# Performance work log

Measured on AMD Instinct MI355X. Metric: run time of the kernel, lower is better.

The kernel has to match this reference:

```python
import jax, jax.numpy as jnp
import numpy as np

B, NF, S, L, H, MID, KS, NC, DENSE = 16, 8, 16, 256, 128, 32, 8, 10, 512
COEFF = 0.1
BN_EPS = 1e-5


def _normalize(x):
    return x / jnp.maximum(jnp.linalg.norm(x, axis=-1, keepdims=True), 1e-12)


def _sparsemax(z):
    # sparsemax over last axis (Martins & Astudillo 2016)
    zs = jnp.flip(jnp.sort(z, axis=-1), axis=-1)
    k = jnp.arange(1, z.shape[-1] + 1, dtype=z.dtype)
    cum = jnp.cumsum(zs, axis=-1)
    support = (1.0 + k * zs) > cum
    ksup = jnp.sum(support, axis=-1, keepdims=True)
    tau = (jnp.take_along_axis(cum, ksup - 1, axis=-1) - 1.0) / ksup.astype(z.dtype)
    return jnp.maximum(z - tau, 0.0)


def _bn_ncl(x, g, b, m, v):  # eval-mode BatchNorm1d on [N, C, L]
    return g[None, :, None] * (x - m[None, :, None]) * jax.lax.rsqrt(v[None, :, None] + BN_EPS) + b[None, :, None]


def _bn_nc(x, g, b, m, v):  # eval-mode BatchNorm1d on [N, C]
    return g * (x - m) * jax.lax.rsqrt(v + BN_EPS) + b


def _conv(x, w, pad):
    return jax.lax.conv_general_dilated(x, w, (1,), [(pad, pad)], dimension_numbers=('NCH', 'OIH', 'NCH'))


def _maxpool2(x):  # MaxPool1d(kernel=2, stride=2, padding=1): -inf padded
    return jax.lax.reduce_window(x, -jnp.inf, jax.lax.max, (1, 1, 2), (1, 1, 2), ((0, 0), (0, 0), (1, 1)))


def _cnn(x, cw1, bn1, cw2, bn2, cw3, bn3):
    x = _maxpool2(jax.nn.relu(_bn_ncl(_conv(x, cw1, KS // 2), *bn1)))
    x = _maxpool2(jax.nn.relu(_bn_ncl(_conv(x, cw2, 4), *bn2)))
    x = _maxpool2(jax.nn.relu(_bn_ncl(_conv(x, cw3, 4), *bn3)))
    return jnp.mean(x, axis=-1)  # AdaptiveAvgPool1d(1) -> [N, H]


def _alpha_beta(x, cw1, bn1, cw2, bn2, cw3, bn3, Wq, bq, Wk, bk, Wv, bv):
    b = x.shape[0]
    xf = jnp.transpose(x, (1, 0, 2, 3)).reshape(NF, b * S, 1, L)
    rep = jax.vmap(_cnn)(xf, cw1, bn1, cw2, bn2, cw3, bn3)  # [F, B*S, H]
    rep = rep.reshape(NF, b, S, H)
    Q = jax.nn.elu(rep @ Wq + bq)
    K = jax.nn.leaky_relu(rep @ Wk + bk)
    V = jax.nn.leaky_relu(rep @ Wv + bv)
    # mean_t(Q @ K^T) == Q @ mean_t(K); then scale by sqrt(d_k)
    scores = jnp.einsum('fbsh,fbh->fbs', Q, jnp.mean(K, axis=2)) / jnp.sqrt(jnp.float32(H))
    intra_aw = _sparsemax(scores)                             # [F, B, S]
    Z = _normalize(jnp.einsum('fbs,fbsh->fbh', intra_aw, V))  # [F, B, H]
    Kn = _normalize(rep)
    inter_scores = jnp.einsum('ibh,fbsh->ifbs', Z, Kn)        # cosine scores (Z already unit-norm)
    inter_aw = _sparsemax(inter_scores)                       # [I, F, B, S]
    U = jnp.einsum('ifbs,fbsh->ibh', inter_aw, rep) / NF      # mean over feature axis f
    Hc = _normalize(jnp.concatenate([Z, U], axis=-1))         # [F, B, 2H]
    feat = jnp.transpose(Hc, (1, 0, 2)).reshape(b, NF * 2 * H)
    return feat, intra_aw, inter_aw


def _forward(src_x, src_y, tgt_x, cw1, bn1_g, bn1_b, bn1_m, bn1_v, cw2, bn2_g, bn2_b, bn2_m, bn2_v, cw3, bn3_g, bn3_b, bn3_m, bn3_v, Wq, bq, Wk, bk, Wv, bv, bnc1_g, bnc1_b, bnc1_m, bnc1_v, W1, b1, bnc2_g, bnc2_b, bnc2_m, bnc2_v, W2, b2):
    bn1 = (bn1_g, bn1_b, bn1_m, bn1_v)
    bn2 = (bn2_g, bn2_b, bn2_m, bn2_v)
    bn3 = (bn3_g, bn3_b, bn3_m, bn3_v)
    sf, sa, sb = _alpha_beta(src_x, cw1, bn1, cw2, bn2, cw3, bn3, Wq, bq, Wk, bk, Wv, bv)
    _, ta, tb = _alpha_beta(tgt_x, cw1, bn1, cw2, bn2, cw3, bn3, Wq, bq, Wk, bk, Wv, bv)
    h = _bn_nc(sf, bnc1_g, bnc1_b, bnc1_m, bnc1_v) @ W1 + b1
    h = jax.nn.leaky_relu(_bn_nc(h, bnc2_g, bnc2_b, bnc2_m, bnc2_v))
    y_pred = jax.nn.softmax(h @ W2 + b2, axis=-1)
    # MMD domain losses (detached in original via torch.tensor(list))
    da = jnp.mean(sa - ta, axis=-2)                           # [F, S]
    loss_a = COEFF * jnp.mean(jnp.linalg.norm(da, axis=-1))
    db = jnp.mean(sb - tb, axis=-2)                           # [I, F, S]
    loss_b = COEFF * jnp.mean(jnp.sqrt(jnp.sum(db * db, axis=(1, 2))))
    dom = jax.lax.stop_gradient(loss_a + loss_b)
    # CrossEntropyLoss applied to already-softmaxed preds, as in source
    logp = jax.nn.log_softmax(y_pred, axis=-1)
    ce = -jnp.mean(logp[jnp.arange(y_pred.shape[0]), src_y])
    return y_pred, ce + dom


def setup_inputs() -> dict:
    ks = jax.random.split(jax.random.key(0), 40)
    rn = lambda i, sh, s=1.0: s * jax.random.normal(ks[i], sh, dtype=jnp.float32)
    ru = lambda i, sh, lo, hi: jax.random.uniform(ks[i], sh, jnp.float32, lo, hi)
    return {
        'src_x': rn(0, (B, NF, S, L)),
        'src_y': jax.random.randint(ks[1], (B,), 0, NC),
        'tgt_x': rn(2, (B, NF, S, L)),
        'cw1': rn(3, (NF, MID, 1, KS), 0.1),
        'bn1_g': ru(4, (NF, MID), 0.75, 1.25), 'bn1_b': rn(5, (NF, MID), 0.1),
        'bn1_m': rn(6, (NF, MID), 0.1), 'bn1_v': ru(7, (NF, MID), 0.5, 1.5),
        'cw2': rn(8, (NF, 2 * MID, MID, 8), 0.05),
        'bn2_g': ru(9, (NF, 2 * MID), 0.75, 1.25), 'bn2_b': rn(10, (NF, 2 * MID), 0.1),
        'bn2_m': rn(11, (NF, 2 * MID), 0.1), 'bn2_v': ru(12, (NF, 2 * MID), 0.5, 1.5),
        'cw3': rn(13, (NF, H, 2 * MID, 8), 0.05),
        'bn3_g': ru(14, (NF, H), 0.75, 1.25), 'bn3_b': rn(15, (NF, H), 0.1),
        'bn3_m': rn(16, (NF, H), 0.1), 'bn3_v': ru(17, (NF, H), 0.5, 1.5),
        'Wq': rn(18, (H, H), 0.05), 'bq': rn(19, (H,), 0.02),
        'Wk': rn(20, (H, H), 0.05), 'bk': rn(21, (H,), 0.02),
        'Wv': rn(22, (H, H), 0.05), 'bv': rn(23, (H,), 0.02),
        'bnc1_g': ru(24, (NF * 2 * H,), 0.75, 1.25), 'bnc1_b': rn(25, (NF * 2 * H,), 0.1),
        'bnc1_m': rn(26, (NF * 2 * H,), 0.1), 'bnc1_v': ru(27, (NF * 2 * H,), 0.5, 1.5),
        'W1': rn(28, (NF * 2 * H, DENSE), 0.03), 'b1': rn(29, (DENSE,), 0.02),
        'bnc2_g': ru(30, (DENSE,), 0.75, 1.25), 'bnc2_b': rn(31, (DENSE,), 0.1),
        'bnc2_m': rn(32, (DENSE,), 0.1), 'bnc2_v': ru(33, (DENSE,), 0.5, 1.5),
        'W2': rn(34, (DENSE, NC), 0.05), 'b2': rn(35, (NC,), 0.02),
    }


def reference(src_x, src_y, tgt_x, cw1, bn1_g, bn1_b, bn1_m, bn1_v, cw2, bn2_g, bn2_b, bn2_m, bn2_v, cw3, bn3_g, bn3_b, bn3_m, bn3_v, Wq, bq, Wk, bk, Wv, bv, bnc1_g, bnc1_b, bnc1_m, bnc1_v, W1, b1, bnc2_g, bnc2_b, bnc2_m, bnc2_v, W2, b2):
    return _forward(src_x, src_y, tgt_x, cw1, bn1_g, bn1_b, bn1_m, bn1_v, cw2, bn2_g, bn2_b, bn2_m, bn2_v, cw3, bn3_g, bn3_b, bn3_m, bn3_v, Wq, bq, Wk, bk, Wv, bv, bnc1_g, bnc1_b, bnc1_m, bnc1_v, W1, b1, bnc2_g, bnc2_b, bnc2_m, bnc2_v, W2, b2)
```

## Files before the change

### kernel.cpp

```cpp
#include <hip/hip_runtime.h>

typedef unsigned short u16;
typedef unsigned int u32;
typedef __attribute__((ext_vector_type(8))) short bfrag;
typedef __attribute__((ext_vector_type(4))) float ffrag;

__device__ __forceinline__ float lrelu(float x) { return x >= 0.f ? x : 0.01f * x; }
__device__ __forceinline__ float eluf(float x)  { return x > 0.f ? x : expm1f(x); }
__device__ __forceinline__ u16 f2bf(float f) {
    u32 x = __float_as_uint(f);
    return (u16)((x + 0x7fffu + ((x >> 16) & 1u)) >> 16);
}
__device__ __forceinline__ u16 f2bt(float f) {
    return (u16)(__float_as_uint(f) >> 16);
}
__device__ __forceinline__ float bf2f(u16 u) {
    return __uint_as_float(((u32)u) << 16);
}

__device__ void sparsemax16(const float* z, float* out) {
    float zs[16];
    for (int i = 0; i < 16; ++i) zs[i] = z[i];
    for (int i = 1; i < 16; ++i) {
        float key = zs[i]; int j = i - 1;
        while (j >= 0 && zs[j] < key) { zs[j + 1] = zs[j]; --j; }
        zs[j + 1] = key;
    }
    float cum[16];
    cum[0] = zs[0];
    for (int i = 1; i < 16; ++i) cum[i] = cum[i - 1] + zs[i];
    int ksup = 0;
    for (int k = 1; k <= 16; ++k)
        if (1.0f + (float)k * zs[k - 1] > cum[k - 1]) ksup++;
    if (ksup < 1) ksup = 1;
    float tau = (cum[ksup - 1] - 1.0f) / (float)ksup;
    for (int i = 0; i < 16; ++i) out[i] = fmaxf(z[i] - tau, 0.0f);
}

__global__ __launch_bounds__(256) void k_wprep(
    const float* __restrict__ w2, const float* __restrict__ w3,
    const float* __restrict__ Wq, const float* __restrict__ Wk,
    const float* __restrict__ Wv,
    u16* __restrict__ wpk2, u16* __restrict__ wpk3, u16* __restrict__ wqkv)
{
    int i = blockIdx.x * 256 + threadIdx.x;
    if (i < 131072) {
        int j = i & 7, L = (i >> 3) & 63, kc = (i >> 9) & 7, nt = (i >> 12) & 3, f = i >> 14;
        int co = nt * 16 + (L & 15);
        int ci = ((L >> 4) << 3) + j;
        wpk2[i] = f2bf(w2[(((size_t)f * 64 + co) * 32 + ci) * 8 + kc]);
    } else if (i < 131072 + 524288) {
        int i2 = i - 131072;
        int j = i2 & 7, L = (i2 >> 3) & 63, kc = (i2 >> 9) & 15, nt = (i2 >> 13) & 7, f = i2 >> 16;
        int co = nt * 16 + (L & 15);
        int ci = ((kc & 1) << 5) + ((L >> 4) << 3) + j;
        wpk3[i2] = f2bf(w3[(((size_t)f * 128 + co) * 64 + ci) * 8 + (kc >> 1)]);
    } else if (i < 131072 + 524288 + 49152) {
        int j2 = i - 655360;
        int proj = j2 >> 14, idx = j2 & 16383;
        int jj = idx & 7, L = (idx >> 3) & 63, kc = (idx >> 9) & 3, nt = idx >> 11;
        int n = nt * 16 + (L & 15);
        int k = kc * 32 + ((L >> 4) << 3) + jj;
        const float* W = proj == 0 ? Wq : (proj == 1 ? Wk : Wv);
        wqkv[j2] = f2bf(W[k * 128 + n]);
    }
}

#define S1T_STRIDE 40
#define S2T_STRIDE 72
#define RB2_STRIDE 68
#define RB3_STRIDE 140
#define RB_OFF 6336
#define SMEM_U16 (RB_OFF + 67 * RB3_STRIDE)

__global__ __launch_bounds__(256) void k_cnn(
    const float* __restrict__ xs, const float* __restrict__ xt,
    const float* __restrict__ w1, const float* __restrict__ g1, const float* __restrict__ b1,
    const float* __restrict__ m1, const float* __restrict__ v1,
    const float* __restrict__ g2, const float* __restrict__ b2,
    const float* __restrict__ m2, const float* __restrict__ v2,
    const float* __restrict__ g3, const float* __restrict__ b3,
    const float* __restrict__ m3, const float* __restrict__ v3,
    const u16* __restrict__ wpk2, const u16* __restrict__ wpk3,
    float* __restrict__ rep)
{
    __shared__ __align__(16) u16 smem[SMEM_U16];
    float* xin = (float*)(smem + RB_OFF);

    int tid = threadIdx.x, blk = blockIdx.x;
    int pass = blk >> 11, f = (blk >> 8) & 7, n = blk & 255;
    int bb = n >> 4, ss = n & 15;
    int lane = tid & 63, w = tid >> 6;
    const float* x = pass ? xt : xs;
    float* rep_p = rep + (size_t)pass * 262144;

    {
        u32* z = (u32*)smem;
        for (int i = tid; i < 80; i += 256) z[i] = 0;
        for (int i = tid; i < 360; i += 256) z[2660 + i] = 0;
        if (tid < 4) { xin[tid] = 0.f; xin[260 + tid] = 0.f; }
        const float* xr = x + (((size_t)bb * 8 + f) * 16 + ss) * 256;
        for (int i = tid; i < 256; i += 256) xin[i + 4] = xr[i];
    }
    __syncthreads();

    if (tid < 208) {
        int cc = tid & 7, jc = tid >> 3;
        int co0 = cc * 4, j0 = jc * 5;
        float wr[4][8];
        for (int c = 0; c < 4; ++c) {
            const float4* q = reinterpret_cast<const float4*>(w1 + ((size_t)f * 32 + co0 + c) * 8);
            float4 a = q[0], bq = q[1];
            wr[c][0] = a.x; wr[c][1] = a.y; wr[c][2] = a.z; wr[c][3] = a.w;
            wr[c][4] = bq.x; wr[c][5] = bq.y; wr[c][6] = bq.z; wr[c][7] = bq.w;
        }
        int px[10];
        for (int i = 0; i < 10; ++i) {
            int p = 2 * j0 - 1 + i;
            px[i] = p < 0 ? 0 : (p > 256 ? 256 : p);
        }
        float acc[4][10];
        for (int c = 0; c < 4; ++c) for (int i = 0; i < 10; ++i) acc[c][i] = 0.f;
        for (int k = 0; k < 8; ++k) {
            float xv[10];
            for (int i = 0; i < 10; ++i) xv[i] = xin[px[i] + k];
            for (int c = 0; c < 4; ++c)
                for (int i = 0; i < 10; ++i) acc[c][i] += wr[c][k] * xv[i];
        }
        for (int c = 0; c < 4; ++c) {
            int co = co0 + c;
            float sc = g1[f * 32 + co] * rsqrtf(v1[f * 32 + co] + 1e-5f);
            float sh = b1[f * 32 + co] - m1[f * 32 + co] * sc;
            for (int jj = 0; jj < 5; ++jj) {
                int j = j0 + jj;
                if (j < 129) {
                    float a0 = fmaxf(acc[c][2 * jj] * sc + sh, 0.f);
                    float a1 = fmaxf(acc[c][2 * jj + 1] * sc + sh, 0.f);
                    smem[(j + 4) * S1T_STRIDE + co] = f2bt(fmaxf(a0, a1));
                }
            }
        }
    }
    __syncthreads();

    {
        int nt = w;
        bfrag B2[8];
        const bfrag* gB = reinterpret_cast<const bfrag*>(wpk2);
        for (int kc = 0; kc < 8; ++kc)
            B2[kc] = gB[(((size_t)f * 4 + nt) * 8 + kc) * 64 + lane];
        int co = nt * 16 + (lane & 15);
        float sc = g2[f * 64 + co] * rsqrtf(v2[f * 64 + co] + 1e-5f);
        float sh = b2[f * 64 + co] - m2[f * 64 + co] * sc;
        int arow = lane & 15, ci0 = (lane >> 4) << 3;
        for (int mt = 0; mt < 9; ++mt) {
            ffrag C = {0.f, 0.f, 0.f, 0.f};
            int rb = mt * 16 + arow;
            for (int kc = 0; kc < 8; ++kc) {
                bfrag A = *reinterpret_cast<const bfrag*>(&smem[(rb + kc) * S1T_STRIDE + ci0]);
                C = __builtin_amdgcn_mfma_f32_16x16x32_bf16(A, B2[kc], C, 0, 0, 0);
            }
            int p0 = mt * 16 + ((lane >> 4) << 2);
            for (int r = 0; r < 4; ++r) {
                int p = p0 + r;
                if (p < 130)
                    smem[RB_OFF + p * RB2_STRIDE + co] = f2bt(fmaxf(C[r] * sc + sh, 0.f));
            }
        }
    }
    __syncthreads();

    {
        u32* z = (u32*)smem;
        for (int i = tid; i < 144; i += 256) z[i] = 0;
        for (int i = tid; i < 612; i += 256) z[2520 + i] = 0;
    }
    for (int e = tid; e < 66 * 64; e += 256) {
        int j = e >> 6, ci = e & 63;
        float vmax;
        if (j == 0) {
            vmax = bf2f(smem[RB_OFF + 0 * RB2_STRIDE + ci]);
        } else if (j == 65) {
            vmax = bf2f(smem[RB_OFF + 129 * RB2_STRIDE + ci]);
        } else {
            float a0 = bf2f(smem[RB_OFF + (2 * j - 1) * RB2_STRIDE + ci]);
            float a1 = bf2f(smem[RB_OFF + (2 * j) * RB2_STRIDE + ci]);
            vmax = fmaxf(a0, a1);
        }
        smem[(j + 4) * S2T_STRIDE + ci] = f2bt(vmax);
    }
    __syncthreads();

    for (int t = 0; t < 2; ++t) {
        int nt = w * 2 + t;
        bfrag B3[16];
        const bfrag* gB = reinterpret_cast<const bfrag*>(wpk3);
        for (int kc = 0; kc < 16; ++kc)
            B3[kc] = gB[(((size_t)f * 8 + nt) * 16 + kc) * 64 + lane];
        int co = nt * 16 + (lane & 15);
        float sc = g3[f * 128 + co] * rsqrtf(v3[f * 128 + co] + 1e-5f);
        float sh = b3[f * 128 + co] - m3[f * 128 + co] * sc;
        int arow = lane & 15, q8 = (lane >> 4) << 3;
        for (int mt = 0; mt < 5; ++mt) {
            ffrag C = {0.f, 0.f, 0.f, 0.f};
            int rb = mt * 16 + arow;
            for (int kc = 0; kc < 16; ++kc) {
                int row = rb + (kc >> 1);
                int ci0 = ((kc & 1) << 5) + q8;
                bfrag A = *reinterpret_cast<const bfrag*>(&smem[row * S2T_STRIDE + ci0]);
                C = __builtin_amdgcn_mfma_f32_16x16x32_bf16(A, B3[kc], C, 0, 0, 0);
            }
            int p0 = mt * 16 + ((lane >> 4) << 2);
            for (int r = 0; r < 4; ++r) {
                int p = p0 + r;
                if (p < 67)
                    smem[RB_OFF + p * RB3_STRIDE + co] = f2bt(fmaxf(C[r] * sc + sh, 0.f));
            }
        }
    }
    __syncthreads();

    if (tid < 128) {
        int co = tid;
        float sum = bf2f(smem[RB_OFF + 0 * RB3_STRIDE + co]);
        for (int j = 1; j < 34; ++j) {
            float a0 = bf2f(smem[RB_OFF + (2 * j - 1) * RB3_STRIDE + co]);
            float a1 = bf2f(smem[RB_OFF + (2 * j) * RB3_STRIDE + co]);
            sum += fmaxf(a0, a1);
        }
        rep_p[(((size_t)f * 256) + n) * 128 + co] = sum * (1.0f / 34.0f);
    }
}

__global__ __launch_bounds__(256) void k_attn1(
    const float* __restrict__ rep, const u16* __restrict__ wqkv,
    const float* __restrict__ bq, const float* __restrict__ bk,
    const float* __restrict__ bv,
    float* __restrict__ Zn, float* __restrict__ rninv, float* __restrict__ iaw)
{
    __shared__ __align__(16) u16 repbf[16 * 136];
    __shared__ float KmL[128], ZL[128], awL[16], scoresL[16], r2L[16];
    __shared__ float spart[4][4][4];
    __shared__ float redL[4];
    int tid = threadIdx.x;
    int pass = blockIdx.x >> 7, f = (blockIdx.x >> 4) & 7, b = blockIdx.x & 15;
    const float* rp = rep + (size_t)pass * 262144 + ((size_t)f * 256 + b * 16) * 128;
    float* Zn_p = Zn + (size_t)pass * 16384;
    float* rninv_p = rninv + (size_t)pass * 2048;
    float* iaw_p = iaw + (size_t)pass * 2048;

    {
        int s = tid >> 4, i = tid & 15, h0 = i * 8;
        const float4* q4 = reinterpret_cast<const float4*>(rp + s * 128 + h0);
        float4 a = q4[0], c = q4[1];
        float p2 = a.x*a.x + a.y*a.y + a.z*a.z + a.w*a.w
                 + c.x*c.x + c.y*c.y + c.z*c.z + c.w*c.w;
        bfrag pk;
        pk[0] = (short)f2bt(a.x); pk[1] = (short)f2bt(a.y);
        pk[2] = (short)f2bt(a.z); pk[3] = (short)f2bt(a.w);
        pk[4] = (short)f2bt(c.x); pk[5] = (short)f2bt(c.y);
        pk[6] = (short)f2bt(c.z); pk[7] = (short)f2bt(c.w);
        *reinterpret_cast<bfrag*>(&repbf[s * 136 + h0]) = pk;
        p2 += __shfl_xor(p2, 1); p2 += __shfl_xor(p2, 2);
        p2 += __shfl_xor(p2, 4); p2 += __shfl_xor(p2, 8);
        if (i == 0) r2L[s] = p2;
    }
    __syncthreads();

    int lane = tid & 63, w = tid >> 6, arow = lane & 15, q = lane >> 4;
    bfrag A[4];
    for (int kc = 0; kc < 4; ++kc)
        A[kc] = *reinterpret_cast<const bfrag*>(&repbf[arow * 136 + kc * 32 + q * 8]);

    float qv[2][4], vvv[2][4];
    int colv[2];
    const bfrag* BB = reinterpret_cast<const bfrag*>(wqkv);
    for (int t = 0; t < 2; ++t) {
        int nt = w * 2 + t;
        ffrag cq = {0.f,0.f,0.f,0.f}, ck = {0.f,0.f,0.f,0.f}, cv = {0.f,0.f,0.f,0.f};
        for (int kc = 0; kc < 4; ++kc) {
            int fi = (nt * 4 + kc) * 64 + lane;
            bfrag Bq = BB[fi];
            bfrag Bk = BB[2048 + fi];
            bfrag Bv = BB[4096 + fi];
            cq = __builtin_amdgcn_mfma_f32_16x16x32_bf16(A[kc], Bq, cq, 0, 0, 0);
            ck = __builtin_amdgcn_mfma_f32_16x16x32_bf16(A[kc], Bk, ck, 0, 0, 0);
            cv = __builtin_amdgcn_mfma_f32_16x16x32_bf16(A[kc], Bv, cv, 0, 0, 0);
        }
        int col = nt * 16 + arow;
        colv[t] = col;
        float bqc = bq[col], bkc = bk[col], bvc = bv[col];
        float kpt = 0.f;
        for (int r = 0; r < 4; ++r) {
            qv[t][r] = eluf(cq[r] + bqc);
            vvv[t][r] = lrelu(cv[r] + bvc);
            kpt += lrelu(ck[r] + bkc);
        }
        kpt += __shfl_xor(kpt, 16);
        kpt += __shfl_xor(kpt, 32);
        if (q == 0) KmL[col] = kpt * (1.f / 16.f);
    }
    __syncthreads();

    {
        float km0 = KmL[colv[0]], km1 = KmL[colv[1]];
        float ps[4];
        for (int r = 0; r < 4; ++r) {
            float v = qv[0][r] * km0 + qv[1][r] * km1;
            v += __shfl_xor(v, 1); v += __shfl_xor(v, 2);
            v += __shfl_xor(v, 4); v += __shfl_xor(v, 8);
            ps[r] = v;
        }
        if (arow == 0)
            for (int r = 0; r < 4; ++r) spart[w][q][r] = ps[r];
    }
    __syncthreads();
    if (tid < 16) {
        int qq = tid >> 2, rr = tid & 3;
        float sc = spart[0][qq][rr] + spart[1][qq][rr] + spart[2][qq][rr] + spart[3][qq][rr];
        scoresL[tid] = sc * 0.08838834764831845f;
        rninv_p[f * 256 + b * 16 + tid] = 1.f / fmaxf(sqrtf(r2L[tid]), 1e-12f);
    }
    __syncthreads();
    if (tid == 0) sparsemax16(scoresL, awL);
    __syncthreads();
    if (tid < 16) iaw_p[f * 256 + b * 16 + tid] = awL[tid];

    for (int t = 0; t < 2; ++t) {
        float zp = 0.f;
        for (int r = 0; r < 4; ++r) zp += awL[q * 4 + r] * vvv[t][r];
        zp += __shfl_xor(zp, 16);
        zp += __shfl_xor(zp, 32);
        if (q == 0) ZL[colv[t]] = zp;
    }
    __syncthreads();
    if (tid < 128) {
        float z = ZL[tid];
        float v = z * z;
        v += __shfl_xor(v, 1); v += __shfl_xor(v, 2); v += __shfl_xor(v, 4);
        v += __shfl_xor(v, 8); v += __shfl_xor(v, 16); v += __shfl_xor(v, 32);
        if (lane == 0) redL[w] = v;
    }
    __syncthreads();
    if (tid == 0) redL[2] = 1.f / fmaxf(sqrtf(redL[0] + redL[1]), 1e-12f);
    __syncthreads();
    if (tid < 128)
        Zn_p[((size_t)f * 16 + b) * 128 + tid] = ZL[tid] * redL[2];
}

__global__ __launch_bounds__(256) void k_attn2(
    const float* __restrict__ rep, const float* __restrict__ Zn,
    const float* __restrict__ rninv, float* __restrict__ ibw,
    const float* __restrict__ g, const float* __restrict__ bb,
    const float* __restrict__ mm, const float* __restrict__ vv,
    float* __restrict__ featbn)
{
    __shared__ float repL[16384];
    __shared__ float ZiL[128], scores[128], UL[128];
    __shared__ float awLf[8][16];
    __shared__ float redL[2];
    int tid = threadIdx.x, blk = blockIdx.x;
    int pass = blk >> 7, b = (blk >> 3) & 15, i = blk & 7;
    const float* rep_p = rep + (size_t)pass * 262144;

    for (int f = 0; f < 8; ++f) {
        const float4* src = reinterpret_cast<const float4*>(
            rep_p + ((size_t)f * 256 + b * 16) * 128);
        float4* dst = reinterpret_cast<float4*>(repL + f * 2048);
        for (int t = tid; t < 512; t += 256) dst[t] = src[t];
    }
    if (tid < 128) ZiL[tid] = Zn[(size_t)pass * 16384 + ((size_t)i * 16 + b) * 128 + tid];
    __syncthreads();

    if (tid < 128) {
        int f = tid >> 4, s = tid & 15;
        const float* rr = repL + tid * 128;
        float a = 0.f;
        for (int h = 0; h < 128; ++h) a += ZiL[h] * rr[h];
        scores[tid] = a * rninv[(size_t)pass * 2048 + f * 256 + b * 16 + s];
    }
    __syncthreads();
    if (tid < 8) {
        float aw[16];
        sparsemax16(&scores[tid * 16], aw);
        for (int s = 0; s < 16; ++s) awLf[tid][s] = aw[s];
    }
    __syncthreads();
    if (tid < 128) {
        int f = tid >> 4, s = tid & 15;
        ibw[(size_t)pass * 16384 + (((size_t)i * 8 + f) * 16 + b) * 16 + s] = awLf[f][s];
    }
    if (pass == 0) {
        if (tid < 128) {
            int h = tid;
            float u = 0.f;
            for (int f = 0; f < 8; ++f) {
                const float* rr = repL + f * 2048 + h;
                const float* aa = awLf[f];
                for (int s = 0; s < 16; ++s) u += aa[s] * rr[s * 128];
            }
            UL[h] = u * 0.125f;
        }
        __syncthreads();
        if (tid < 128) {
            int lane = tid & 63, w = tid >> 6;
            float v = ZiL[tid] * ZiL[tid] + UL[tid] * UL[tid];
            v += __shfl_xor(v, 1); v += __shfl_xor(v, 2); v += __shfl_xor(v, 4);
            v += __shfl_xor(v, 8); v += __shfl_xor(v, 16); v += __shfl_xor(v, 32);
            if (lane == 0) redL[w] = v;
        }
        __syncthreads();
        if (tid < 256) {
            float inv = 1.f / fmaxf(sqrtf(redL[0] + redL[1]), 1e-12f);
            int d = tid;
            int e = i * 256 + d;
            float val = (d < 128 ? ZiL[d] : UL[d - 128]) * inv;
            float scv = g[e] * rsqrtf(vv[e] + 1e-5f);
            featbn[b * 2048 + e] = (val - mm[e]) * scv + bb[e];
        }
    }
}

__global__ __launch_bounds__(256) void k_head1(
    const float* __restrict__ featbn,
    const float* __restrict__ W1, const float* __restrict__ b1,
    const float* __restrict__ g2, const float* __restrict__ bb2,
    const float* __restrict__ mm2, const float* __restrict__ vv2,
    float* __restrict__ h2ws)
{
    __shared__ float featL[2048];
    __shared__ float part[32][32];
    int tid = threadIdx.x, blk = blockIdx.x;
    int b = blk >> 4, cc = blk & 15;
    {
        const float4* src = reinterpret_cast<const float4*>(featbn + b * 2048);
        float4* dst = reinterpret_cast<float4*>(featL);
        for (int i = tid; i < 512; i += 256) dst[i] = src[i];
    }
    __syncthreads();
    int ks = tid >> 3, cg = tid & 7;
    int col0 = cc * 32 + cg * 4;
    float4 acc = {0.f, 0.f, 0.f, 0.f};
    const float* fl = featL + ks * 64;
    for (int c = 0; c < 64; ++c) {
        int k = ks * 64 + c;
        float4 wv = *reinterpret_cast<const float4*>(W1 + (size_t)k * 512 + col0);
        float fv = fl[c];
        acc.x += fv * wv.x; acc.y += fv * wv.y;
        acc.z += fv * wv.z; acc.w += fv * wv.w;
    }
    part[ks][cg * 4 + 0] = acc.x;
    part[ks][cg * 4 + 1] = acc.y;
    part[ks][cg * 4 + 2] = acc.z;
    part[ks][cg * 4 + 3] = acc.w;
    __syncthreads();
    if (tid < 32) {
        int colw = cc * 32 + tid;
        float s = b1[colw];
        for (int k2 = 0; k2 < 32; ++k2) s += part[k2][tid];
        float scv = g2[colw] * rsqrtf(vv2[colw] + 1e-5f);
        float val = (s - mm2[colw]) * scv + bb2[colw];
        h2ws[b * 512 + colw] = lrelu(val);
    }
}

__global__ __launch_bounds__(256) void k_tail(
    const float* __restrict__ h2ws,
    const float* __restrict__ W2, const float* __restrict__ b2,
    const float* __restrict__ sa, const float* __restrict__ ta,
    const float* __restrict__ sb, const float* __restrict__ tb,
    const int* __restrict__ sy, float* __restrict__ dout)
{
    __shared__ float h2L[8192];
    __shared__ float lgL[160], ypL[160];
    __shared__ float sA[8], sB[8];
    int tid = threadIdx.x;
    for (int i = tid; i < 8192; i += 256) h2L[i] = h2ws[i];
    if (tid < 8) { sA[tid] = 0.f; sB[tid] = 0.f; }
    __syncthreads();
    if (tid < 160) {
        int b = tid / 10, j = tid - b * 10;
        float a = b2[j];
        const float* h = h2L + b * 512;
        for (int c = 0; c < 512; ++c) a += h[c] * W2[c * 10 + j];
        lgL[tid] = a;
    }
    __syncthreads();
    if (tid < 16) {
        int b = tid;
        float mx = lgL[b * 10];
        for (int j = 1; j < 10; ++j) mx = fmaxf(mx, lgL[b * 10 + j]);
        float sum = 0.f, ex[10];
        for (int j = 0; j < 10; ++j) { ex[j] = expf(lgL[b * 10 + j] - mx); sum += ex[j]; }
        for (int j = 0; j < 10; ++j) {
            float p = ex[j] / sum;
            ypL[b * 10 + j] = p;
            dout[b * 10 + j] = p;
        }
    }
    __syncthreads();
    if (tid < 128) {
        int f = tid >> 4, s = tid & 15;
        float d = 0.f;
        for (int b = 0; b < 16; ++b) d += sa[f * 256 + b * 16 + s] - ta[f * 256 + b * 16 + s];
        d *= (1.f / 16.f);
        atomicAdd(&sA[f], d * d);
    }
    for (int e = tid; e < 1024; e += 256) {
        int i = e >> 7, f = (e >> 4) & 7, s = e & 15;
        float d = 0.f;
        int base = ((i * 8 + f) * 16) * 16 + s;
        for (int b = 0; b < 16; ++b) d += sb[base + b * 16] - tb[base + b * 16];
        d *= (1.f / 16.f);
        atomicAdd(&sB[i], d * d);
    }
    __syncthreads();
    if (tid == 0) {
        float la = 0.f, lb = 0.f;
        for (int f = 0; f < 8; ++f) la += sqrtf(sA[f]);
        for (int i = 0; i < 8; ++i) lb += sqrtf(sB[i]);
        la *= 0.1f / 8.f;
        lb *= 0.1f / 8.f;
        float ce = 0.f;
        for (int b = 0; b < 16; ++b) {
            const float* y = ypL + b * 10;
            float mx = y[0];
            for (int j = 1; j < 10; ++j) mx = fmaxf(mx, y[j]);
            float sum = 0.f;
            for (int j = 0; j < 10; ++j) sum += expf(y[j] - mx);
            float lse = mx + logf(sum);
            ce += lse - y[sy[b]];
        }
        ce *= (1.f / 16.f);
        dout[160] = ce + la + lb;
    }
}

extern "C" void kernel_launch(void* const* d_in, const int* in_sizes, int n_in,
                              void* d_out, int out_size, void* d_ws, size_t ws_size,
                              hipStream_t stream) {
    (void)in_sizes; (void)n_in; (void)out_size; (void)ws_size;
    const float* src_x = (const float*)d_in[0];
    const int*   src_y = (const int*)d_in[1];
    const float* tgt_x = (const float*)d_in[2];
    const float *cw1 = (const float*)d_in[3], *bn1g = (const float*)d_in[4],
                *bn1b = (const float*)d_in[5], *bn1m = (const float*)d_in[6],
                *bn1v = (const float*)d_in[7];
    const float *cw2 = (const float*)d_in[8], *bn2g = (const float*)d_in[9],
                *bn2b = (const float*)d_in[10], *bn2m = (const float*)d_in[11],
                *bn2v = (const float*)d_in[12];
    const float *cw3 = (const float*)d_in[13], *bn3g = (const float*)d_in[14],
                *bn3b = (const float*)d_in[15], *bn3m = (const float*)d_in[16],
                *bn3v = (const float*)d_in[17];
    const float *Wq = (const float*)d_in[18], *bq = (const float*)d_in[19],
                *Wk = (const float*)d_in[20], *bk = (const float*)d_in[21],
                *Wv = (const float*)d_in[22], *bv = (const float*)d_in[23];
    const float *bc1g = (const float*)d_in[24], *bc1b = (const float*)d_in[25],
                *bc1m = (const float*)d_in[26], *bc1v = (const float*)d_in[27];
    const float *W1 = (const float*)d_in[28], *b1 = (const float*)d_in[29];
    const float *bc2g = (const float*)d_in[30], *bc2b = (const float*)d_in[31],
                *bc2m = (const float*)d_in[32], *bc2v = (const float*)d_in[33];
    const float *W2 = (const float*)d_in[34], *b2 = (const float*)d_in[35];

    float* ws = (float*)d_ws;
    size_t o = 0;
    float* rep    = ws + o; o += (size_t)2 * 262144;
    float* Zn     = ws + o; o += (size_t)2 * 16384;
    float* rninv  = ws + o; o += (size_t)2 * 2048;
    float* ia     = ws + o; o += (size_t)2 * 2048;
    float* ib     = ws + o; o += (size_t)2 * 16384;
    float* featbn = ws + o; o += (size_t)16 * 2048;
    float* h2ws   = ws + o; o += (size_t)16 * 512;
    u16* wpk2 = (u16*)(ws + o); o += 65536;
    u16* wpk3 = (u16*)(ws + o); o += 262144;
    u16* wqkv = (u16*)(ws + o); o += 24576;

    k_wprep<<<2752, 256, 0, stream>>>(cw2, cw3, Wq, Wk, Wv, wpk2, wpk3, wqkv);
    k_cnn<<<4096, 256, 0, stream>>>(src_x, tgt_x,
        cw1, bn1g, bn1b, bn1m, bn1v,
        bn2g, bn2b, bn2m, bn2v,
        bn3g, bn3b, bn3m, bn3v,
        wpk2, wpk3, rep);
    k_attn1<<<256, 256, 0, stream>>>(rep, wqkv, bq, bk, bv, Zn, rninv, ia);
    k_attn2<<<256, 256, 0, stream>>>(rep, Zn, rninv, ib, bc1g, bc1b, bc1m, bc1v, featbn);
    k_head1<<<256, 256, 0, stream>>>(featbn, W1, b1, bc2g, bc2b, bc2m, bc2v, h2ws);
    k_tail<<<1, 256, 0, stream>>>(h2ws, W2, b2, ia, ia + 2048, ib, ib + 16384,
                                  src_y, (float*)d_out);
}
```

Before: 311.6 us.

## Fuse post-CNN kernels into one persistent kernel with atomic grid barriers

Merges the four post-CNN kernels (attention 1, attention 2, head dense layer, tail loss) into one 256-block kernel. The stages are separated by software grid barriers built on an agent-scope atomic counter, which k_wprep resets. This removes three kernel launch gaps and their drain and refill time. In exchange, all 256 blocks must be resident at once, each block now holds about 67KB of shared memory, and the spin-waits add their own latency.

```diff
diff --git a/kernel.cpp b/kernel.cpp
--- a/kernel.cpp
+++ b/kernel.cpp
@@ -37,13 +37,31 @@
     for (int i = 0; i < 16; ++i) out[i] = fmaxf(z[i] - tau, 0.0f);
 }
 
+__device__ __forceinline__ void grid_arrive(u32* ctr) {
+    __syncthreads();
+    if (threadIdx.x == 0)
+        __hip_atomic_fetch_add(ctr, 1u, __ATOMIC_ACQ_REL, __HIP_MEMORY_SCOPE_AGENT);
+}
+__device__ __forceinline__ void grid_wait(u32* ctr, u32 target) {
+    if (threadIdx.x == 0) {
+        u32 v;
+        do {
+            __builtin_amdgcn_s_sleep(2);
+            v = __hip_atomic_load(ctr, __ATOMIC_ACQUIRE, __HIP_MEMORY_SCOPE_AGENT);
+        } while (v < target);
+    }
+    __syncthreads();
+}
+
 __global__ __launch_bounds__(256) void k_wprep(
     const float* __restrict__ w2, const float* __restrict__ w3,
     const float* __restrict__ Wq, const float* __restrict__ Wk,
     const float* __restrict__ Wv,
-    u16* __restrict__ wpk2, u16* __restrict__ wpk3, u16* __restrict__ wqkv)
+    u16* __restrict__ wpk2, u16* __restrict__ wpk3, u16* __restrict__ wqkv,
+    u32* __restrict__ bar)
 {
     int i = blockIdx.x * 256 + threadIdx.x;
+    if (i == 0) *bar = 0;
     if (i < 131072) {
         int j = i & 7, L = (i >> 3) & 63, kc = (i >> 9) & 7, nt = (i >> 12) & 3, f = i >> 14;
         int co = nt * 16 + (L & 15);
@@ -232,307 +250,325 @@
     }
 }
 
-__global__ __launch_bounds__(256) void k_attn1(
+__global__ __launch_bounds__(256) void k_post(
     const float* __restrict__ rep, const u16* __restrict__ wqkv,
     const float* __restrict__ bq, const float* __restrict__ bk,
     const float* __restrict__ bv,
-    float* __restrict__ Zn, float* __restrict__ rninv, float* __restrict__ iaw)
+    float* __restrict__ Zn, float* __restrict__ rninv,
+    float* __restrict__ iaw, float* __restrict__ ibw,
+    const float* __restrict__ gC, const float* __restrict__ bC,
+    const float* __restrict__ mC, const float* __restrict__ vC,
+    float* __restrict__ featbn,
+    const float* __restrict__ W1, const float* __restrict__ b1d,
+    const float* __restrict__ g2c, const float* __restrict__ bb2,
+    const float* __restrict__ mm2, const float* __restrict__ vv2,
+    float* __restrict__ h2ws,
+    const float* __restrict__ W2, const float* __restrict__ b2d,
+    const int* __restrict__ sy, float* __restrict__ dout,
+    u32* __restrict__ bar)
 {
-    __shared__ __align__(16) u16 repbf[16 * 136];
-    __shared__ float KmL[128], ZL[128], awL[16], scoresL[16], r2L[16];
-    __shared__ float spart[4][4][4];
-    __shared__ float redL[4];
-    int tid = threadIdx.x;
-    int pass = blockIdx.x >> 7, f = (blockIdx.x >> 4) & 7, b = blockIdx.x & 15;
-    const float* rp = rep + (size_t)pass * 262144 + ((size_t)f * 256 + b * 16) * 128;
-    float* Zn_p = Zn + (size_t)pass * 16384;
-    float* rninv_p = rninv + (size_t)pass * 2048;
-    float* iaw_p = iaw + (size_t)pass * 2048;
+    __shared__ __align__(16) unsigned char sbuf[67600];
+    int tid = threadIdx.x, blk = blockIdx.x;
+    int lane = tid & 63, w = tid >> 6;
 
     {
-        int s = tid >> 4, i = tid & 15, h0 = i * 8;
-        const float4* q4 = reinterpret_cast<const float4*>(rp + s * 128 + h0);
-        float4 a = q4[0], c = q4[1];
-        float p2 = a.x*a.x + a.y*a.y + a.z*a.z + a.w*a.w
-                 + c.x*c.x + c.y*c.y + c.z*c.z + c.w*c.w;
-        bfrag pk;
-        pk[0] = (short)f2bt(a.x); pk[1] = (short)f2bt(a.y);
-        pk[2] = (short)f2bt(a.z); pk[3] = (short)f2bt(a.w);
-        pk[4] = (short)f2bt(c.x); pk[5] = (short)f2bt(c.y);
-        pk[6] = (short)f2bt(c.z); pk[7] = (short)f2bt(c.w);
-        *reinterpret_cast<bfrag*>(&repbf[s * 136 + h0]) = pk;
-        p2 += __shfl_xor(p2, 1); p2 += __shfl_xor(p2, 2);
-        p2 += __shfl_xor(p2, 4); p2 += __shfl_xor(p2, 8);
-        if (i == 0) r2L[s] = p2;
-    }
-    __syncthreads();
-
-    int lane = tid & 63, w = tid >> 6, arow = lane & 15, q = lane >> 4;
-    bfrag A[4];
-    for (int kc = 0; kc < 4; ++kc)
-        A[kc] = *reinterpret_cast<const bfrag*>(&repbf[arow * 136 + kc * 32 + q * 8]);
-
-    float qv[2][4], vvv[2][4];
-    int colv[2];
-    const bfrag* BB = reinterpret_cast<const bfrag*>(wqkv);
-    for (int t = 0; t < 2; ++t) {
-        int nt = w * 2 + t;
-        ffrag cq = {0.f,0.f,0.f,0.f}, ck = {0.f,0.f,0.f,0.f}, cv = {0.f,0.f,0.f,0.f};
-        for (int kc = 0; kc < 4; ++kc) {
-            int fi = (nt * 4 + kc) * 64 + lane;
-            bfrag Bq = BB[fi];
-            bfrag Bk = BB[2048 + fi];
-            bfrag Bv = BB[4096 + fi];
-            cq = __builtin_amdgcn_mfma_f32_16x16x32_bf16(A[kc], Bq, cq, 0, 0, 0);
-            ck = __builtin_amdgcn_mfma_f32_16x16x32_bf16(A[kc], Bk, ck, 0, 0, 0);
-            cv = __builtin_amdgcn_mfma_f32_16x16x32_bf16(A[kc], Bv, cv, 0, 0, 0);
-        }
-        int col = nt * 16 + arow;
-        colv[t] = col;
-        float bqc = bq[col], bkc = bk[col], bvc = bv[col];
-        float kpt = 0.f;
-        for (int r = 0; r < 4; ++r) {
-            qv[t][r] = eluf(cq[r] + bqc);
-            vvv[t][r] = lrelu(cv[r] + bvc);
-            kpt += lrelu(ck[r] + bkc);
-        }
-        kpt += __shfl_xor(kpt, 16);
-        kpt += __shfl_xor(kpt, 32);
-        if (q == 0) KmL[col] = kpt * (1.f / 16.f);
-    }
-    __syncthreads();
-
-    {
-        float km0 = KmL[colv[0]], km1 = KmL[colv[1]];
-        float ps[4];
-        for (int r = 0; r < 4; ++r) {
-            float v = qv[0][r] * km0 + qv[1][r] * km1;
-            v += __shfl_xor(v, 1); v += __shfl_xor(v, 2);
-            v += __shfl_xor(v, 4); v += __shfl_xor(v, 8);
-            ps[r] = v;
-        }
-        if (arow == 0)
-            for (int r = 0; r < 4; ++r) spart[w][q][r] = ps[r];
-    }
-    __syncthreads();
-    if (tid < 16) {
-        int qq = tid >> 2, rr = tid & 3;
-        float sc = spart[0][qq][rr] + spart[1][qq][rr] + spart[2][qq][rr] + spart[3][qq][rr];
-        scoresL[tid] = sc * 0.08838834764831845f;
-        rninv_p[f * 256 + b * 16 + tid] = 1.f / fmaxf(sqrtf(r2L[tid]), 1e-12f);
-    }
-    __syncthreads();
-    if (tid == 0) sparsemax16(scoresL, awL);
-    __syncthreads();
-    if (tid < 16) iaw_p[f * 256 + b * 16 + tid] = awL[tid];
-
-    for (int t = 0; t < 2; ++t) {
-        float zp = 0.f;
-        for (int r = 0; r < 4; ++r) zp += awL[q * 4 + r] * vvv[t][r];
-        zp += __shfl_xor(zp, 16);
-        zp += __shfl_xor(zp, 32);
-        if (q == 0) ZL[colv[t]] = zp;
-    }
-    __syncthreads();
-    if (tid < 128) {
-        float z = ZL[tid];
-        float v = z * z;
-        v += __shfl_xor(v, 1); v += __shfl_xor(v, 2); v += __shfl_xor(v, 4);
-        v += __shfl_xor(v, 8); v += __shfl_xor(v, 16); v += __shfl_xor(v, 32);
-        if (lane == 0) redL[w] = v;
-    }
-    __syncthreads();
-    if (tid == 0) redL[2] = 1.f / fmaxf(sqrtf(redL[0] + redL[1]), 1e-12f);
-    __syncthreads();
-    if (tid < 128)
-        Zn_p[((size_t)f * 16 + b) * 128 + tid] = ZL[tid] * redL[2];
-}
-
-__global__ __launch_bounds__(256) void k_attn2(
-    const float* __restrict__ rep, const float* __restrict__ Zn,
-    const float* __restrict__ rninv, float* __restrict__ ibw,
-    const float* __restrict__ g, const float* __restrict__ bb,
-    const float* __restrict__ mm, const float* __restrict__ vv,
-    float* __restrict__ featbn)
-{
-    __shared__ float repL[16384];
-    __shared__ float ZiL[128], scores[128], UL[128];
-    __shared__ float awLf[8][16];
-    __shared__ float redL[2];
-    int tid = threadIdx.x, blk = blockIdx.x;
-    int pass = blk >> 7, b = (blk >> 3) & 15, i = blk & 7;
-    const float* rep_p = rep + (size_t)pass * 262144;
-
-    for (int f = 0; f < 8; ++f) {
-        const float4* src = reinterpret_cast<const float4*>(
-            rep_p + ((size_t)f * 256 + b * 16) * 128);
-        float4* dst = reinterpret_cast<float4*>(repL + f * 2048);
-        for (int t = tid; t < 512; t += 256) dst[t] = src[t];
-    }
-    if (tid < 128) ZiL[tid] = Zn[(size_t)pass * 16384 + ((size_t)i * 16 + b) * 128 + tid];
-    __syncthreads();
-
-    if (tid < 128) {
-        int f = tid >> 4, s = tid & 15;
-        const float* rr = repL + tid * 128;
-        float a = 0.f;
-        for (int h = 0; h < 128; ++h) a += ZiL[h] * rr[h];
-        scores[tid] = a * rninv[(size_t)pass * 2048 + f * 256 + b * 16 + s];
-    }
-    __syncthreads();
-    if (tid < 8) {
-        float aw[16];
-        sparsemax16(&scores[tid * 16], aw);
-        for (int s = 0; s < 16; ++s) awLf[tid][s] = aw[s];
-    }
-    __syncthreads();
-    if (tid < 128) {
-        int f = tid >> 4, s = tid & 15;
-        ibw[(size_t)pass * 16384 + (((size_t)i * 8 + f) * 16 + b) * 16 + s] = awLf[f][s];
-    }
-    if (pass == 0) {
+        u16* repbf = (u16*)sbuf;
+        float* KmL = (float*)(sbuf + 4352);
+        float* ZL = KmL + 128;
+        float* awL = ZL + 128;
+        float* scoresL = awL + 16;
+        float* r2L = scoresL + 16;
+        float* spart = r2L + 16;
+        float* redL = spart + 64;
+
+        int pass = blk >> 7, f = (blk >> 4) & 7, b = blk & 15;
+        const float* rp = rep + (size_t)pass * 262144 + ((size_t)f * 256 + b * 16) * 128;
+        float* Zn_p = Zn + (size_t)pass * 16384;
+        float* rninv_p = rninv + (size_t)pass * 2048;
+        float* iaw_p = iaw + (size_t)pass * 2048;
+
+        {
+            int s = tid >> 4, i = tid & 15, h0 = i * 8;
+            const float4* q4 = reinterpret_cast<const float4*>(rp + s * 128 + h0);
+            float4 a = q4[0], c = q4[1];
+            float p2 = a.x*a.x + a.y*a.y + a.z*a.z + a.w*a.w
+                     + c.x*c.x + c.y*c.y + c.z*c.z + c.w*c.w;
+            bfrag pk;
+            pk[0] = (short)f2bt(a.x); pk[1] = (short)f2bt(a.y);
+            pk[2] = (short)f2bt(a.z); pk[3] = (short)f2bt(a.w);
+            pk[4] = (short)f2bt(c.x); pk[5] = (short)f2bt(c.y);
+            pk[6] = (short)f2bt(c.z); pk[7] = (short)f2bt(c.w);
+            *reinterpret_cast<bfrag*>(&repbf[s * 136 + h0]) = pk;
+            p2 += __shfl_xor(p2, 1); p2 += __shfl_xor(p2, 2);
+            p2 += __shfl_xor(p2, 4); p2 += __shfl_xor(p2, 8);
+            if (i == 0) r2L[s] = p2;
+        }
+        __syncthreads();
+
+        int arow = lane & 15, q = lane >> 4;
+        bfrag A[4];
+        for (int kc = 0; kc < 4; ++kc)
+            A[kc] = *reinterpret_cast<const bfrag*>(&repbf[arow * 136 + kc * 32 + q * 8]);
+
+        float qv[2][4], vvv[2][4];
+        int colv[2];
+        const bfrag* BB = reinterpret_cast<const bfrag*>(wqkv);
+        for (int t = 0; t < 2; ++t) {
+            int nt = w * 2 + t;
+            ffrag cq = {0.f,0.f,0.f,0.f}, ck = {0.f,0.f,0.f,0.f}, cv = {0.f,0.f,0.f,0.f};
+            for (int kc = 0; kc < 4; ++kc) {
+                int fi = (nt * 4 + kc) * 64 + lane;
+                bfrag Bq = BB[fi];
+                bfrag Bk = BB[2048 + fi];
+                bfrag Bv = BB[4096 + fi];
+                cq = __builtin_amdgcn_mfma_f32_16x16x32_bf16(A[kc], Bq, cq, 0, 0, 0);
+                ck = __builtin_amdgcn_mfma_f32_16x16x32_bf16(A[kc], Bk, ck, 0, 0, 0);
+                cv = __builtin_amdgcn_mfma_f32_16x16x32_bf16(A[kc], Bv, cv, 0, 0, 0);
+            }
+            int col = nt * 16 + arow;
+            colv[t] = col;
+            float bqc = bq[col], bkc = bk[col], bvc = bv[col];
+            float kpt = 0.f;
+            for (int r = 0; r < 4; ++r) {
+                qv[t][r] = eluf(cq[r] + bqc);
+                vvv[t][r] = lrelu(cv[r] + bvc);
+                kpt += lrelu(ck[r] + bkc);
+            }
+            kpt += __shfl_xor(kpt, 16);
+            kpt += __shfl_xor(kpt, 32);
+            if (q == 0) KmL[col] = kpt * (1.f / 16.f);
+        }
+        __syncthreads();
+
+        {
+            float km0 = KmL[colv[0]], km1 = KmL[colv[1]];
+            float ps[4];
+            for (int r = 0; r < 4; ++r) {
+                float v = qv[0][r] * km0 + qv[1][r] * km1;
+                v += __shfl_xor(v, 1); v += __shfl_xor(v, 2);
+                v += __shfl_xor(v, 4); v += __shfl_xor(v, 8);
+                ps[r] = v;
+            }
+            if (arow == 0)
+                for (int r = 0; r < 4; ++r) spart[w * 16 + q * 4 + r] = ps[r];
+        }
+        __syncthreads();
+        if (tid < 16) {
+            int qq = tid >> 2, rr = tid & 3;
+            float sc = spart[0 * 16 + qq * 4 + rr] + spart[1 * 16 + qq * 4 + rr]
+                     + spart[2 * 16 + qq * 4 + rr] + spart[3 * 16 + qq * 4 + rr];
+            scoresL[tid] = sc * 0.08838834764831845f;
+            rninv_p[f * 256 + b * 16 + tid] = 1.f / fmaxf(sqrtf(r2L[tid]), 1e-12f);
+        }
+        __syncthreads();
+        if (tid == 0) sparsemax16(scoresL, awL);
+        __syncthreads();
+        if (tid < 16) iaw_p[f * 256 + b * 16 + tid] = awL[tid];
+
+        for (int t = 0; t < 2; ++t) {
+            float zp = 0.f;
+            for (int r = 0; r < 4; ++r) zp += awL[q * 4 + r] * vvv[t][r];
+            zp += __shfl_xor(zp, 16);
+            zp += __shfl_xor(zp, 32);
+            if (q == 0) ZL[colv[t]] = zp;
+        }
+        __syncthreads();
         if (tid < 128) {
-            int h = tid;
-            float u = 0.f;
-            for (int f = 0; f < 8; ++f) {
-                const float* rr = repL + f * 2048 + h;
-                const float* aa = awLf[f];
-                for (int s = 0; s < 16; ++s) u += aa[s] * rr[s * 128];
-            }
-            UL[h] = u * 0.125f;
-        }
-        __syncthreads();
-        if (tid < 128) {
-            int lane = tid & 63, w = tid >> 6;
-            float v = ZiL[tid] * ZiL[tid] + UL[tid] * UL[tid];
+            float z = ZL[tid];
+            float v = z * z;
             v += __shfl_xor(v, 1); v += __shfl_xor(v, 2); v += __shfl_xor(v, 4);
             v += __shfl_xor(v, 8); v += __shfl_xor(v, 16); v += __shfl_xor(v, 32);
             if (lane == 0) redL[w] = v;
         }
         __syncthreads();
-        if (tid < 256) {
-            float inv = 1.f / fmaxf(sqrtf(redL[0] + redL[1]), 1e-12f);
-            int d = tid;
-            int e = i * 256 + d;
-            float val = (d < 128 ? ZiL[d] : UL[d - 128]) * inv;
-            float scv = g[e] * rsqrtf(vv[e] + 1e-5f);
-            featbn[b * 2048 + e] = (val - mm[e]) * scv + bb[e];
-        }
-    }
-}
-
-__global__ __launch_bounds__(256) void k_head1(
-    const float* __restrict__ featbn,
-    const float* __restrict__ W1, const float* __restrict__ b1,
-    const float* __restrict__ g2, const float* __restrict__ bb2,
-    const float* __restrict__ mm2, const float* __restrict__ vv2,
-    float* __restrict__ h2ws)
-{
-    __shared__ float featL[2048];
-    __shared__ float part[32][32];
-    int tid = threadIdx.x, blk = blockIdx.x;
-    int b = blk >> 4, cc = blk & 15;
+        if (tid == 0) redL[2] = 1.f / fmaxf(sqrtf(redL[0] + redL[1]), 1e-12f);
+        __syncthreads();
+        if (tid < 128)
+            Zn_p[((size_t)f * 16 + b) * 128 + tid] = ZL[tid] * redL[2];
+    }
+    grid_arrive(bar);
+    grid_wait(bar, 256);
+
     {
-        const float4* src = reinterpret_cast<const float4*>(featbn + b * 2048);
-        float4* dst = reinterpret_cast<float4*>(featL);
-        for (int i = tid; i < 512; i += 256) dst[i] = src[i];
-    }
-    __syncthreads();
-    int ks = tid >> 3, cg = tid & 7;
-    int col0 = cc * 32 + cg * 4;
-    float4 acc = {0.f, 0.f, 0.f, 0.f};
-    const float* fl = featL + ks * 64;
-    for (int c = 0; c < 64; ++c) {
-        int k = ks * 64 + c;
-        float4 wv = *reinterpret_cast<const float4*>(W1 + (size_t)k * 512 + col0);
-        float fv = fl[c];
-        acc.x += fv * wv.x; acc.y += fv * wv.y;
-        acc.z += fv * wv.z; acc.w += fv * wv.w;
-    }
-    part[ks][cg * 4 + 0] = acc.x;
-    part[ks][cg * 4 + 1] = acc.y;
-    part[ks][cg * 4 + 2] = acc.z;
-    part[ks][cg * 4 + 3] = acc.w;
-    __syncthreads();
-    if (tid < 32) {
-        int colw = cc * 32 + tid;
-        float s = b1[colw];
-        for (int k2 = 0; k2 < 32; ++k2) s += part[k2][tid];
-        float scv = g2[colw] * rsqrtf(vv2[colw] + 1e-5f);
-        float val = (s - mm2[colw]) * scv + bb2[colw];
-        h2ws[b * 512 + colw] = lrelu(val);
-    }
-}
-
-__global__ __launch_bounds__(256) void k_tail(
-    const float* __restrict__ h2ws,
-    const float* __restrict__ W2, const float* __restrict__ b2,
-    const float* __restrict__ sa, const float* __restrict__ ta,
-    const float* __restrict__ sb, const float* __restrict__ tb,
-    const int* __restrict__ sy, float* __restrict__ dout)
-{
-    __shared__ float h2L[8192];
-    __shared__ float lgL[160], ypL[160];
-    __shared__ float sA[8], sB[8];
-    int tid = threadIdx.x;
-    for (int i = tid; i < 8192; i += 256) h2L[i] = h2ws[i];
-    if (tid < 8) { sA[tid] = 0.f; sB[tid] = 0.f; }
-    __syncthreads();
-    if (tid < 160) {
-        int b = tid / 10, j = tid - b * 10;
-        float a = b2[j];
-        const float* h = h2L + b * 512;
-        for (int c = 0; c < 512; ++c) a += h[c] * W2[c * 10 + j];
-        lgL[tid] = a;
-    }
-    __syncthreads();
-    if (tid < 16) {
-        int b = tid;
-        float mx = lgL[b * 10];
-        for (int j = 1; j < 10; ++j) mx = fmaxf(mx, lgL[b * 10 + j]);
-        float sum = 0.f, ex[10];
-        for (int j = 0; j < 10; ++j) { ex[j] = expf(lgL[b * 10 + j] - mx); sum += ex[j]; }
-        for (int j = 0; j < 10; ++j) {
-            float p = ex[j] / sum;
-            ypL[b * 10 + j] = p;
-            dout[b * 10 + j] = p;
-        }
-    }
-    __syncthreads();
-    if (tid < 128) {
-        int f = tid >> 4, s = tid & 15;
-        float d = 0.f;
-        for (int b = 0; b < 16; ++b) d += sa[f * 256 + b * 16 + s] - ta[f * 256 + b * 16 + s];
-        d *= (1.f / 16.f);
-        atomicAdd(&sA[f], d * d);
-    }
-    for (int e = tid; e < 1024; e += 256) {
-        int i = e >> 7, f = (e >> 4) & 7, s = e & 15;
-        float d = 0.f;
-        int base = ((i * 8 + f) * 16) * 16 + s;
-        for (int b = 0; b < 16; ++b) d += sb[base + b * 16] - tb[base + b * 16];
-        d *= (1.f / 16.f);
-        atomicAdd(&sB[i], d * d);
-    }
-    __syncthreads();
-    if (tid == 0) {
-        float la = 0.f, lb = 0.f;
-        for (int f = 0; f < 8; ++f) la += sqrtf(sA[f]);
-        for (int i = 0; i < 8; ++i) lb += sqrtf(sB[i]);
-        la *= 0.1f / 8.f;
-        lb *= 0.1f / 8.f;
-        float ce = 0.f;
-        for (int b = 0; b < 16; ++b) {
-            const float* y = ypL + b * 10;
-            float mx = y[0];
-            for (int j = 1; j < 10; ++j) mx = fmaxf(mx, y[j]);
-            float sum = 0.f;
-            for (int j = 0; j < 10; ++j) sum += expf(y[j] - mx);
-            float lse = mx + logf(sum);
-            ce += lse - y[sy[b]];
-        }
-        ce *= (1.f / 16.f);
-        dout[160] = ce + la + lb;
+        float* repL = (float*)sbuf;
+        float* ZiL = (float*)(sbuf + 65536);
+        float* scores = ZiL + 128;
+        float* UL = scores + 128;
+        float* awLf = UL + 128;
+        float* redB = awLf + 128;
+
+        int pass = blk >> 7, b = (blk >> 3) & 15, i = blk & 7;
+        const float* rep_p = rep + (size_t)pass * 262144;
+
+        for (int f = 0; f < 8; ++f) {
+            const float4* src = reinterpret_cast<const float4*>(
+                rep_p + ((size_t)f * 256 + b * 16) * 128);
+            float4* dst = reinterpret_cast<float4*>(repL + f * 2048);
+            for (int t = tid; t < 512; t += 256) dst[t] = src[t];
+        }
+        if (tid < 128) ZiL[tid] = Zn[(size_t)pass * 16384 + ((size_t)i * 16 + b) * 128 + tid];
+        __syncthreads();
+
+        if (tid < 128) {
+            int f = tid >> 4, s = tid & 15;
+            const float* rr = repL + tid * 128;
+            float a = 0.f;
+            for (int h = 0; h < 128; ++h) a += ZiL[h] * rr[h];
+            scores[tid] = a * rninv[(size_t)pass * 2048 + f * 256 + b * 16 + s];
+        }
+        __syncthreads();
+        if (tid < 8) {
+            float aw[16];
+            sparsemax16(&scores[tid * 16], aw);
+            for (int s = 0; s < 16; ++s) awLf[tid * 16 + s] = aw[s];
+        }
+        __syncthreads();
+        if (tid < 128) {
+            int f = tid >> 4, s = tid & 15;
+            ibw[(size_t)pass * 16384 + (((size_t)i * 8 + f) * 16 + b) * 16 + s] = awLf[f * 16 + s];
+        }
+        if (pass == 0) {
+            if (tid < 128) {
+                int h = tid;
+                float u = 0.f;
+                for (int f = 0; f < 8; ++f) {
+                    const float* rr = repL + f * 2048 + h;
+                    const float* aa = awLf + f * 16;
+                    for (int s = 0; s < 16; ++s) u += aa[s] * rr[s * 128];
+                }
+                UL[h] = u * 0.125f;
+            }
+            __syncthreads();
+            if (tid < 128) {
+                float v = ZiL[tid] * ZiL[tid] + UL[tid] * UL[tid];
+                v += __shfl_xor(v, 1); v += __shfl_xor(v, 2); v += __shfl_xor(v, 4);
+                v += __shfl_xor(v, 8); v += __shfl_xor(v, 16); v += __shfl_xor(v, 32);
+                if (lane == 0) redB[w] = v;
+            }
+            __syncthreads();
+            {
+                float inv = 1.f / fmaxf(sqrtf(redB[0] + redB[1]), 1e-12f);
+                int d = tid;
+                int e = i * 256 + d;
+                float val = (d < 128 ? ZiL[d] : UL[d - 128]) * inv;
+                float scv = gC[e] * rsqrtf(vC[e] + 1e-5f);
+                featbn[b * 2048 + e] = (val - mC[e]) * scv + bC[e];
+            }
+        }
+    }
+    grid_arrive(bar);
+    grid_wait(bar, 512);
+
+    {
+        float* featL = (float*)sbuf;
+        float* part = featL + 2048;
+
+        int b = blk >> 4, cc = blk & 15;
+        {
+            const float4* src = reinterpret_cast<const float4*>(featbn + b * 2048);
+            float4* dst = reinterpret_cast<float4*>(featL);
+            for (int i = tid; i < 512; i += 256) dst[i] = src[i];
+        }
+        __syncthreads();
+        int ks = tid >> 3, cg = tid & 7;
+        int col0 = cc * 32 + cg * 4;
+        float4 acc = {0.f, 0.f, 0.f, 0.f};
+        const float* fl = featL + ks * 64;
+        for (int c = 0; c < 64; ++c) {
+            int k = ks * 64 + c;
+            float4 wv = *reinterpret_cast<const float4*>(W1 + (size_t)k * 512 + col0);
+            float fv = fl[c];
+            acc.x += fv * wv.x; acc.y += fv * wv.y;
+            acc.z += fv * wv.z; acc.w += fv * wv.w;
+        }
+        part[ks * 32 + cg * 4 + 0] = acc.x;
+        part[ks * 32 + cg * 4 + 1] = acc.y;
+        part[ks * 32 + cg * 4 + 2] = acc.z;
+        part[ks * 32 + cg * 4 + 3] = acc.w;
+        __syncthreads();
+        if (tid < 32) {
+            int colw = cc * 32 + tid;
+            float s = b1d[colw];
+            for (int k2 = 0; k2 < 32; ++k2) s += part[k2 * 32 + tid];
+            float scv = g2c[colw] * rsqrtf(vv2[colw] + 1e-5f);
+            float val = (s - mm2[colw]) * scv + bb2[colw];
+            h2ws[b * 512 + colw] = lrelu(val);
+        }
+    }
+    grid_arrive(bar);
+    if (blk != 0) return;
+    grid_wait(bar, 768);
+
+    {
+        float* h2L = (float*)sbuf;
+        float* lgL = h2L + 8192;
+        float* ypL = lgL + 160;
+        float* sA = ypL + 160;
+        float* sB = sA + 8;
+        const float* sa = iaw;
+        const float* ta = iaw + 2048;
+        const float* sbp = ibw;
+        const float* tbp = ibw + 16384;
+
+        for (int i = tid; i < 8192; i += 256) h2L[i] = h2ws[i];
+        if (tid < 8) { sA[tid] = 0.f; sB[tid] = 0.f; }
+        __syncthreads();
+        if (tid < 160) {
+            int b = tid / 10, j = tid - b * 10;
+            float a = b2d[j];
+            const float* h = h2L + b * 512;
+            for (int c = 0; c < 512; ++c) a += h[c] * W2[c * 10 + j];
+            lgL[tid] = a;
+        }
+        __syncthreads();
+        if (tid < 16) {
+            int b = tid;
+            float mx = lgL[b * 10];
+            for (int j = 1; j < 10; ++j) mx = fmaxf(mx, lgL[b * 10 + j]);
+            float sum = 0.f, ex[10];
+            for (int j = 0; j < 10; ++j) { ex[j] = expf(lgL[b * 10 + j] - mx); sum += ex[j]; }
+            for (int j = 0; j < 10; ++j) {
+                float p = ex[j] / sum;
+                ypL[b * 10 + j] = p;
+                dout[b * 10 + j] = p;
+            }
+        }
+        __syncthreads();
+        if (tid < 128) {
+            int f = tid >> 4, s = tid & 15;
+            float d = 0.f;
+            for (int b = 0; b < 16; ++b) d += sa[f * 256 + b * 16 + s] - ta[f * 256 + b * 16 + s];
+            d *= (1.f / 16.f);
+            atomicAdd(&sA[f], d * d);
+        }
+        for (int e = tid; e < 1024; e += 256) {
+            int i = e >> 7, f = (e >> 4) & 7, s = e & 15;
+            float d = 0.f;
+            int base = ((i * 8 + f) * 16) * 16 + s;
+            for (int b = 0; b < 16; ++b) d += sbp[base + b * 16] - tbp[base + b * 16];
+            d *= (1.f / 16.f);
+            atomicAdd(&sB[i], d * d);
+        }
+        __syncthreads();
+        if (tid == 0) {
+            float la = 0.f, lb = 0.f;
+            for (int f = 0; f < 8; ++f) la += sqrtf(sA[f]);
+            for (int i = 0; i < 8; ++i) lb += sqrtf(sB[i]);
+            la *= 0.1f / 8.f;
+            lb *= 0.1f / 8.f;
+            float ce = 0.f;
+            for (int b = 0; b < 16; ++b) {
+                const float* y = ypL + b * 10;
+                float mx = y[0];
+                for (int j = 1; j < 10; ++j) mx = fmaxf(mx, y[j]);
+                float sum = 0.f;
+                for (int j = 0; j < 10; ++j) sum += expf(y[j] - mx);
+                float lse = mx + logf(sum);
+                ce += lse - y[sy[b]];
+            }
+            ce *= (1.f / 16.f);
+            dout[160] = ce + la + lb;
+        }
     }
 }
 
@@ -574,16 +610,16 @@
     u16* wpk2 = (u16*)(ws + o); o += 65536;
     u16* wpk3 = (u16*)(ws + o); o += 262144;
     u16* wqkv = (u16*)(ws + o); o += 24576;
-
-    k_wprep<<<2752, 256, 0, stream>>>(cw2, cw3, Wq, Wk, Wv, wpk2, wpk3, wqkv);
+    u32* bar  = (u32*)(ws + o); o += 16;
+
+    k_wprep<<<2752, 256, 0, stream>>>(cw2, cw3, Wq, Wk, Wv, wpk2, wpk3, wqkv, bar);
     k_cnn<<<4096, 256, 0, stream>>>(src_x, tgt_x,
         cw1, bn1g, bn1b, bn1m, bn1v,
         bn2g, bn2b, bn2m, bn2v,
         bn3g, bn3b, bn3m, bn3v,
         wpk2, wpk3, rep);
-    k_attn1<<<256, 256, 0, stream>>>(rep, wqkv, bq, bk, bv, Zn, rninv, ia);
-    k_attn2<<<256, 256, 0, stream>>>(rep, Zn, rninv, ib, bc1g, bc1b, bc1m, bc1v, featbn);
-    k_head1<<<256, 256, 0, stream>>>(featbn, W1, b1, bc2g, bc2b, bc2m, bc2v, h2ws);
-    k_tail<<<1, 256, 0, stream>>>(h2ws, W2, b2, ia, ia + 2048, ib, ib + 16384,
-                                  src_y, (float*)d_out);
-}
+    k_post<<<256, 256, 0, stream>>>(rep, wqkv, bq, bk, bv, Zn, rninv, ia, ib,
+                                    bc1g, bc1b, bc1m, bc1v, featbn,
+                                    W1, b1, bc2g, bc2b, bc2m, bc2v, h2ws,
+                                    W2, b2, src_y, (float*)d_out, bar);
+}
```

Result: slower. 371.4 us (+19.2%).
